# Kernel tuning notes

Measured on AMD Instinct MI355X. Metric: run time of the kernel, lower is better.

## Reference

```python
import jax, jax.numpy as jnp
import numpy as np

# Static SMPL kinematic tree (24 joints)
PARENTS = [-1, 0, 0, 0, 1, 2, 3, 4, 5, 6, 7, 8, 9, 9, 9, 12, 13, 14, 16, 17, 18, 19, 20, 21]
NJ = 24      # num joints
FS = 6       # local_feature_size
NF = 7       # bone_dim (1) + FS


def _topo_order(parents):
    children = {i: [] for i in range(len(parents))}
    roots = []
    for i, p in enumerate(parents):
        (roots if p == -1 else children[p]).append(i)
    order = []
    queue = roots[:]
    while queue:
        c = queue.pop(0)
        order.append(c)
        queue.extend(sorted(children[c]))
    return order

TOPO = _topo_order(PARENTS)


def setup_inputs() -> dict:
    key = jax.random.key(0)
    ks = jax.random.split(key, 5)
    B = 524288
    x = jax.random.normal(ks[0], (B, NJ, 1), dtype=jnp.float32)
    s = 1.0 / np.sqrt(NF)
    # Stacked per-joint weights. For the root joint, the parent-feature rows of
    # W1 are multiplied by a zero virtual parent feature, which is exactly
    # equivalent to the original Linear(1, 7) root MLP.
    W1 = jax.random.uniform(ks[1], (NJ, NF, NF), jnp.float32, -s, s)
    b1 = jax.random.uniform(ks[2], (NJ, NF), jnp.float32, -s, s)
    W2 = jax.random.uniform(ks[3], (NJ, NF, FS), jnp.float32, -s, s)
    b2 = jax.random.uniform(ks[4], (NJ, FS), jnp.float32, -s, s)
    return {"x": x, "W1": W1, "b1": b1, "W2": W2, "b2": b2}


def reference(x, W1, b1, W2, b2):
    # x: [B, NJ, 1]; sequential propagation over the fixed kinematic tree.
    B = x.shape[0]
    feats = [None] * NJ
    zero_pf = jnp.zeros((B, FS), x.dtype)
    for i in TOPO:
        p = PARENTS[i]
        pf = zero_pf if p == -1 else feats[p]
        inp = jnp.concatenate([x[:, i, :], pf], axis=-1)  # [B, 7]
        h = jax.nn.relu(inp @ W1[i] + b1[i])               # [B, 7]
        feats[i] = jax.nn.relu(h @ W2[i] + b2[i])          # [B, 6]
    return jnp.concatenate(feats, axis=-1)                 # [B, 144]
```

## Files before the change

### kernel.cpp

```cpp
#include <hip/hip_runtime.h>

#define NJ 24
#define NF 7
#define FS 6
#define THREADS 256
#define CUNITS 12
#define PAD 13

typedef float v4f __attribute__((ext_vector_type(4)));

__device__ constexpr int kParents[NJ] = {-1, 0, 0, 0, 1, 2, 3, 4, 5, 6, 7, 8,
                                          9, 9, 9, 12, 13, 14, 16, 17, 18, 19, 20, 21};

#define JOINT(i)                                                              \
    {                                                                         \
        const int p_ = kParents[i];                                           \
        float inp_[NF];                                                       \
        inp_[0] = xr[i];                                                      \
        _Pragma("unroll")                                                     \
        for (int j = 0; j < FS; ++j)                                          \
            inp_[1 + j] = (p_ < 0) ? 0.0f : feats[(p_ < 0) ? 0 : p_][j];      \
        float h_[NF];                                                         \
        _Pragma("unroll")                                                     \
        for (int j = 0; j < NF; ++j) h_[j] = b1[(i) * NF + j];                \
        _Pragma("unroll")                                                     \
        for (int k = 0; k < NF; ++k) {                                        \
            const float a_ = inp_[k];                                         \
            _Pragma("unroll")                                                 \
            for (int j = 0; j < NF; ++j)                                      \
                h_[j] = fmaf(a_, W1[(i) * NF * NF + k * NF + j], h_[j]);      \
        }                                                                     \
        _Pragma("unroll")                                                     \
        for (int j = 0; j < NF; ++j) h_[j] = fmaxf(h_[j], 0.0f);              \
        float f_[FS];                                                         \
        _Pragma("unroll")                                                     \
        for (int j = 0; j < FS; ++j) f_[j] = b2[(i) * FS + j];                \
        _Pragma("unroll")                                                     \
        for (int k = 0; k < NF; ++k) {                                        \
            const float a_ = h_[k];                                           \
            _Pragma("unroll")                                                 \
            for (int j = 0; j < FS; ++j)                                      \
                f_[j] = fmaf(a_, W2[(i) * NF * FS + k * FS + j], f_[j]);      \
        }                                                                     \
        _Pragma("unroll")                                                     \
        for (int j = 0; j < FS; ++j) {                                        \
            f_[j] = fmaxf(f_[j], 0.0f);                                       \
            feats[i][j] = f_[j];                                              \
        }                                                                     \
        if ((i) & 1) {                                                        \
            const int pp_ = ((i) >> 1) & 3;                                   \
            v4f* st_ = myStage + pp_ * 3;                                     \
            st_[0] = (v4f){feats[(i) - 1][0], feats[(i) - 1][1],              \
                           feats[(i) - 1][2], feats[(i) - 1][3]};             \
            st_[1] = (v4f){feats[(i) - 1][4], feats[(i) - 1][5],              \
                           f_[0], f_[1]};                                     \
            st_[2] = (v4f){f_[2], f_[3], f_[4], f_[5]};                       \
        }                                                                     \
    }

#define FLUSH(C)                                                              \
    {                                                                         \
        _Pragma("unroll")                                                     \
        for (int j = 0; j < CUNITS; ++j) {                                    \
            const int G = j * 64 + lane;                                      \
            const int s = G / CUNITS;                                         \
            const int q = G - s * CUNITS;                                     \
            fr[j] = sm[wid][s * PAD + q];                                     \
        }                                                                     \
        _Pragma("unroll")                                                     \
        for (int j = 0; j < CUNITS; ++j) {                                    \
            v4f* dst_ = reinterpret_cast<v4f*>(                               \
                reinterpret_cast<char*>(obase) + voff[j] + (C) * 192);        \
            *dst_ = fr[j];                                                    \
        }                                                                     \
    }

#define KEEP12(A)                                                             \
    asm volatile("" :: "v"(A[0]), "v"(A[1]), "v"(A[2]), "v"(A[3]),            \
                 "v"(A[4]), "v"(A[5]), "v"(A[6]), "v"(A[7]),                  \
                 "v"(A[8]), "v"(A[9]), "v"(A[10]), "v"(A[11]));

__global__ __launch_bounds__(THREADS, 3) void se1d_kernel(
    const float* __restrict__ x,
    const float* __restrict__ W1,
    const float* __restrict__ b1,
    const float* __restrict__ W2,
    const float* __restrict__ b2,
    float* __restrict__ out, int B)
{
    __shared__ v4f sm[THREADS / 64][64 * PAD];

    const int t    = threadIdx.x;
    const int lane = t & 63;
    const int wid  = __builtin_amdgcn_readfirstlane(threadIdx.x >> 6);
    const int b    = blockIdx.x * THREADS + t;
    const int wb   = blockIdx.x * THREADS + wid * 64;

    v4f* const myStage = &sm[wid][lane * PAD];
    v4f* const obase = reinterpret_cast<v4f*>(out) + (size_t)wb * 36;

    int voff[CUNITS];
    #pragma unroll
    for (int j = 0; j < CUNITS; ++j) {
        const int G = j * 64 + lane;
        const int s = G / CUNITS;
        const int q = G - s * CUNITS;
        voff[j] = (s * 36 + q) * 16;
    }

    float xr[NJ];
    {
        const v4f* xv = reinterpret_cast<const v4f*>(x + (size_t)b * NJ);
        #pragma unroll
        for (int c = 0; c < NJ / 4; ++c) {
            v4f v = __builtin_nontemporal_load(xv + c);
            xr[c * 4 + 0] = v.x; xr[c * 4 + 1] = v.y;
            xr[c * 4 + 2] = v.z; xr[c * 4 + 3] = v.w;
        }
    }

    float feats[NJ][FS];
    v4f fr[CUNITS];

    JOINT(0) JOINT(1) JOINT(2) JOINT(3) JOINT(4) JOINT(5) JOINT(6) JOINT(7)
    FLUSH(0);
    JOINT(8) JOINT(9) JOINT(10) JOINT(11)
    JOINT(12) JOINT(13) JOINT(14) JOINT(15)
    FLUSH(1);
    JOINT(16) JOINT(17) JOINT(18) JOINT(19)
    JOINT(20) JOINT(21) JOINT(22) JOINT(23)
    FLUSH(2);

    KEEP12(fr);
    (void)B;
}

extern "C" void kernel_launch(void* const* d_in, const int* in_sizes, int n_in,
                              void* d_out, int out_size, void* d_ws, size_t ws_size,
                              hipStream_t stream) {
    const float* x  = (const float*)d_in[0];
    const float* W1 = (const float*)d_in[1];
    const float* b1 = (const float*)d_in[2];
    const float* W2 = (const float*)d_in[3];
    const float* b2 = (const float*)d_in[4];
    float* out = (float*)d_out;
    const int B = in_sizes[0] / NJ;
    const int grid = B / THREADS;
    hipLaunchKernelGGL(se1d_kernel, dim3(grid), dim3(THREADS), 0, stream,
                       x, W1, b1, W2, b2, out, B);
}
```

Baseline: 102.3 us.

## Process two batch rows per thread to share weight loads and raise ILP

Each thread now computes two independent batch elements (A and B), halving the block size to 128 threads while keeping 256 rows per block. Each scalar weight load is reused for two FMAs, and the two independent dependency chains give more instruction-level parallelism. Output stores become nontemporal. The cost is roughly double the register footprint (two feature arrays, two staging sets) and a lower occupancy hint of 2, which may cause spills or leave too few waves to hide memory latency.

```diff
diff --git a/kernel.cpp b/kernel.cpp
--- a/kernel.cpp
+++ b/kernel.cpp
@@ -3,7 +3,7 @@
 #define NJ 24
 #define NF 7
 #define FS 6
-#define THREADS 256
+#define THREADS 128
 #define CUNITS 12
 #define PAD 13
 
@@ -12,67 +12,90 @@
 __device__ constexpr int kParents[NJ] = {-1, 0, 0, 0, 1, 2, 3, 4, 5, 6, 7, 8,
                                           9, 9, 9, 12, 13, 14, 16, 17, 18, 19, 20, 21};
 
-#define JOINT(i)                                                              \
+#define JOINT2(i)                                                             \
     {                                                                         \
         const int p_ = kParents[i];                                           \
-        float inp_[NF];                                                       \
-        inp_[0] = xr[i];                                                      \
+        float inA_[NF], inB_[NF];                                             \
+        inA_[0] = xrA[i]; inB_[0] = xrB[i];                                   \
         _Pragma("unroll")                                                     \
-        for (int j = 0; j < FS; ++j)                                          \
-            inp_[1 + j] = (p_ < 0) ? 0.0f : feats[(p_ < 0) ? 0 : p_][j];      \
-        float h_[NF];                                                         \
+        for (int j = 0; j < FS; ++j) {                                        \
+            inA_[1 + j] = (p_ < 0) ? 0.0f : fA[(p_ < 0) ? 0 : p_][j];         \
+            inB_[1 + j] = (p_ < 0) ? 0.0f : fB[(p_ < 0) ? 0 : p_][j];         \
+        }                                                                     \
+        float hA_[NF], hB_[NF];                                               \
         _Pragma("unroll")                                                     \
-        for (int j = 0; j < NF; ++j) h_[j] = b1[(i) * NF + j];                \
+        for (int j = 0; j < NF; ++j) {                                        \
+            const float bv_ = b1[(i) * NF + j];                               \
+            hA_[j] = bv_; hB_[j] = bv_;                                       \
+        }                                                                     \
         _Pragma("unroll")                                                     \
         for (int k = 0; k < NF; ++k) {                                        \
-            const float a_ = inp_[k];                                         \
+            const float aA_ = inA_[k], aB_ = inB_[k];                         \
             _Pragma("unroll")                                                 \
-            for (int j = 0; j < NF; ++j)                                      \
-                h_[j] = fmaf(a_, W1[(i) * NF * NF + k * NF + j], h_[j]);      \
+            for (int j = 0; j < NF; ++j) {                                    \
+                const float w_ = W1[(i) * NF * NF + k * NF + j];              \
+                hA_[j] = fmaf(aA_, w_, hA_[j]);                               \
+                hB_[j] = fmaf(aB_, w_, hB_[j]);                               \
+            }                                                                 \
         }                                                                     \
         _Pragma("unroll")                                                     \
-        for (int j = 0; j < NF; ++j) h_[j] = fmaxf(h_[j], 0.0f);              \
-        float f_[FS];                                                         \
+        for (int j = 0; j < NF; ++j) {                                        \
+            hA_[j] = fmaxf(hA_[j], 0.0f); hB_[j] = fmaxf(hB_[j], 0.0f);       \
+        }                                                                     \
+        float fA_[FS], fB_[FS];                                               \
         _Pragma("unroll")                                                     \
-        for (int j = 0; j < FS; ++j) f_[j] = b2[(i) * FS + j];                \
+        for (int j = 0; j < FS; ++j) {                                        \
+            const float bv_ = b2[(i) * FS + j];                               \
+            fA_[j] = bv_; fB_[j] = bv_;                                       \
+        }                                                                     \
         _Pragma("unroll")                                                     \
         for (int k = 0; k < NF; ++k) {                                        \
-            const float a_ = h_[k];                                           \
+            const float aA_ = hA_[k], aB_ = hB_[k];                           \
             _Pragma("unroll")                                                 \
-            for (int j = 0; j < FS; ++j)                                      \
-                f_[j] = fmaf(a_, W2[(i) * NF * FS + k * FS + j], f_[j]);      \
+            for (int j = 0; j < FS; ++j) {                                    \
+                const float w_ = W2[(i) * NF * FS + k * FS + j];              \
+                fA_[j] = fmaf(aA_, w_, fA_[j]);                               \
+                fB_[j] = fmaf(aB_, w_, fB_[j]);                               \
+            }                                                                 \
         }                                                                     \
         _Pragma("unroll")                                                     \
         for (int j = 0; j < FS; ++j) {                                        \
-            f_[j] = fmaxf(f_[j], 0.0f);                                       \
-            feats[i][j] = f_[j];                                              \
+            fA_[j] = fmaxf(fA_[j], 0.0f); fA[i][j] = fA_[j];                  \
+            fB_[j] = fmaxf(fB_[j], 0.0f); fB[i][j] = fB_[j];                  \
         }                                                                     \
-        if ((i) & 1) {                                                        \
+        if ((i) & 1) {              \
             const int pp_ = ((i) >> 1) & 3;                                   \
-            v4f* st_ = myStage + pp_ * 3;                                     \
-            st_[0] = (v4f){feats[(i) - 1][0], feats[(i) - 1][1],              \
-                           feats[(i) - 1][2], feats[(i) - 1][3]};             \
-            st_[1] = (v4f){feats[(i) - 1][4], feats[(i) - 1][5],              \
-                           f_[0], f_[1]};                                     \
-            st_[2] = (v4f){f_[2], f_[3], f_[4], f_[5]};                       \
+            v4f* sA_ = myStageA + pp_ * 3;                                    \
+            sA_[0] = (v4f){fA[(i) - 1][0], fA[(i) - 1][1],                    \
+                           fA[(i) - 1][2], fA[(i) - 1][3]};                   \
+            sA_[1] = (v4f){fA[(i) - 1][4], fA[(i) - 1][5], fA_[0], fA_[1]};   \
+            sA_[2] = (v4f){fA_[2], fA_[3], fA_[4], fA_[5]};                   \
+            v4f* sB_ = myStageB + pp_ * 3;                                    \
+            sB_[0] = (v4f){fB[(i) - 1][0], fB[(i) - 1][1],                    \
+                           fB[(i) - 1][2], fB[(i) - 1][3]};                   \
+            sB_[1] = (v4f){fB[(i) - 1][4], fB[(i) - 1][5], fB_[0], fB_[1]};   \
+            sB_[2] = (v4f){fB_[2], fB_[3], fB_[4], fB_[5]};                   \
         }                                                                     \
     }
 
-#define FLUSH(C)                                                              \
+#define FLUSHAB(C)                                                            \
     {                                                                         \
         _Pragma("unroll")                                                     \
         for (int j = 0; j < CUNITS; ++j) {                                    \
             const int G = j * 64 + lane;                                      \
             const int s = G / CUNITS;                                         \
             const int q = G - s * CUNITS;                                     \
-            fr[j] = sm[wid][s * PAD + q];                                     \
+            frA[j] = smA[s * PAD + q];                                        \
+            frB[j] = smB[s * PAD + q];                                        \
         }                                                                     \
         _Pragma("unroll")                                                     \
-        for (int j = 0; j < CUNITS; ++j) {                                    \
-            v4f* dst_ = reinterpret_cast<v4f*>(                               \
-                reinterpret_cast<char*>(obase) + voff[j] + (C) * 192);        \
-            *dst_ = fr[j];                                                    \
-        }                                                                     \
+        for (int j = 0; j < CUNITS; ++j)                                      \
+            __builtin_nontemporal_store(frA[j], reinterpret_cast<v4f*>(       \
+                obaseA + voff[j] + (C) * 192));                               \
+        _Pragma("unroll")                                                     \
+        for (int j = 0; j < CUNITS; ++j)                                      \
+            __builtin_nontemporal_store(frB[j], reinterpret_cast<v4f*>(       \
+                obaseB + voff[j] + (C) * 192));                               \
     }
 
 #define KEEP12(A)                                                             \
@@ -80,7 +103,7 @@
                  "v"(A[4]), "v"(A[5]), "v"(A[6]), "v"(A[7]),                  \
                  "v"(A[8]), "v"(A[9]), "v"(A[10]), "v"(A[11]));
 
-__global__ __launch_bounds__(THREADS, 3) void se1d_kernel(
+__global__ __launch_bounds__(THREADS, 2) void se1d_kernel(
     const float* __restrict__ x,
     const float* __restrict__ W1,
     const float* __restrict__ b1,
@@ -88,16 +111,25 @@
     const float* __restrict__ b2,
     float* __restrict__ out, int B)
 {
-    __shared__ v4f sm[THREADS / 64][64 * PAD];
+    __shared__ v4f sm[2][2][64 * PAD];
 
     const int t    = threadIdx.x;
     const int lane = t & 63;
     const int wid  = __builtin_amdgcn_readfirstlane(threadIdx.x >> 6);
-    const int b    = blockIdx.x * THREADS + t;
-    const int wb   = blockIdx.x * THREADS + wid * 64;
+    const int base = blockIdx.x * 256;
+    const int bA   = base + wid * 64 + lane;
+    const int bB   = base + 128 + wid * 64 + lane;
+    const int wbA  = base + wid * 64;
+    const int wbB  = base + 128 + wid * 64;
 
-    v4f* const myStage = &sm[wid][lane * PAD];
-    v4f* const obase = reinterpret_cast<v4f*>(out) + (size_t)wb * 36;
+    v4f* const myStageA = &sm[wid][0][lane * PAD];
+    v4f* const myStageB = &sm[wid][1][lane * PAD];
+    v4f* const smA = sm[wid][0];
+    v4f* const smB = sm[wid][1];
+    char* const obaseA = reinterpret_cast<char*>(
+        reinterpret_cast<v4f*>(out) + (size_t)wbA * 36);
+    char* const obaseB = reinterpret_cast<char*>(
+        reinterpret_cast<v4f*>(out) + (size_t)wbB * 36);
 
     int voff[CUNITS];
     #pragma unroll
@@ -108,30 +140,36 @@
         voff[j] = (s * 36 + q) * 16;
     }
 
-    float xr[NJ];
+    float xrA[NJ], xrB[NJ];
     {
-        const v4f* xv = reinterpret_cast<const v4f*>(x + (size_t)b * NJ);
+        const v4f* xvA = reinterpret_cast<const v4f*>(x + (size_t)bA * NJ);
+        const v4f* xvB = reinterpret_cast<const v4f*>(x + (size_t)bB * NJ);
         #pragma unroll
         for (int c = 0; c < NJ / 4; ++c) {
-            v4f v = __builtin_nontemporal_load(xv + c);
-            xr[c * 4 + 0] = v.x; xr[c * 4 + 1] = v.y;
-            xr[c * 4 + 2] = v.z; xr[c * 4 + 3] = v.w;
+            v4f a = __builtin_nontemporal_load(xvA + c);
+            v4f b = __builtin_nontemporal_load(xvB + c);
+            xrA[c * 4 + 0] = a.x; xrA[c * 4 + 1] = a.y;
+            xrA[c * 4 + 2] = a.z; xrA[c * 4 + 3] = a.w;
+            xrB[c * 4 + 0] = b.x; xrB[c * 4 + 1] = b.y;
+            xrB[c * 4 + 2] = b.z; xrB[c * 4 + 3] = b.w;
         }
     }
 
-    float feats[NJ][FS];
-    v4f fr[CUNITS];
+    float fA[NJ][FS], fB[NJ][FS];
+    v4f frA[CUNITS], frB[CUNITS];
 
-    JOINT(0) JOINT(1) JOINT(2) JOINT(3) JOINT(4) JOINT(5) JOINT(6) JOINT(7)
-    FLUSH(0);
-    JOINT(8) JOINT(9) JOINT(10) JOINT(11)
-    JOINT(12) JOINT(13) JOINT(14) JOINT(15)
-    FLUSH(1);
-    JOINT(16) JOINT(17) JOINT(18) JOINT(19)
-    JOINT(20) JOINT(21) JOINT(22) JOINT(23)
-    FLUSH(2);
+    JOINT2(0) JOINT2(1) JOINT2(2) JOINT2(3)
+    JOINT2(4) JOINT2(5) JOINT2(6) JOINT2(7)
+    FLUSHAB(0);
+    JOINT2(8) JOINT2(9) JOINT2(10) JOINT2(11)
+    JOINT2(12) JOINT2(13) JOINT2(14) JOINT2(15)
+    FLUSHAB(1);
+    JOINT2(16) JOINT2(17) JOINT2(18) JOINT2(19)
+    JOINT2(20) JOINT2(21) JOINT2(22) JOINT2(23)
+    FLUSHAB(2);
 
-    KEEP12(fr);
+    KEEP12(frA);
+    KEEP12(frB);
     (void)B;
 }
 
@@ -145,7 +183,7 @@
     const float* b2 = (const float*)d_in[4];
     float* out = (float*)d_out;
     const int B = in_sizes[0] / NJ;
-    const int grid = B / THREADS;
+    const int grid = B / 256;
     hipLaunchKernelGGL(se1d_kernel, dim3(grid), dim3(THREADS), 0, stream,
                        x, W1, b1, W2, b2, out, B);
 }
```

Result: slower. 107.2 us (+4.8%).
